# Kernel optimization log

Hardware: AMD Instinct MI355X
Metric: run time of the kernel (lower is better)

The kernel has to match this reference:

```python
import jax, jax.numpy as jnp
import numpy as np

NQ, NK, D = 8192, 8192, 256
NEG_INF = -1e30


def setup_inputs() -> dict:
    key = jax.random.key(0)
    kK, kV, kQ, kM = jax.random.split(key, 4)
    K = jax.random.normal(kK, (NK, D), dtype=jnp.float32)
    V = jax.random.normal(kV, (NK, D), dtype=jnp.float32)
    Q = jax.random.normal(kQ, (NQ, D), dtype=jnp.float32)
    m = jax.random.randint(kM, (NQ, NK), 0, 2) > 0  # bool mask, True = attend
    return {"K": K, "V": V, "Q": Q, "m": m}


def reference(K, V, Q, m):
    # affinity: scaled dot product with optional mask
    scale = 1.0 / jnp.sqrt(jnp.asarray(D, dtype=Q.dtype))
    QKt = jnp.einsum('qd,kd->qk', Q, K) * scale  # [NQ, NK]
    QKt = jnp.where(m, QKt, NEG_INF)
    # normalization: softmax over keys
    QKt_n = jax.nn.softmax(QKt, axis=-1)
    # weighted sum of values
    return QKt_n @ V  # [NQ, D]
```

## Files before the change

### kernel.cpp

```cpp
#include <hip/hip_runtime.h>
#include <stdint.h>
#include <stddef.h>

#define NQS 8192
#define NKS 8192
#define DS  256

typedef _Float16 half8 __attribute__((ext_vector_type(8)));
typedef _Float16 half4v __attribute__((ext_vector_type(4)));
typedef float floatx16 __attribute__((ext_vector_type(16)));
typedef float floatx4e __attribute__((ext_vector_type(4)));
typedef uint32_t uint32x4 __attribute__((ext_vector_type(4)));

#define MFMA32(A,B,C) __builtin_amdgcn_mfma_f32_32x32x16_f16(A,B,C,0,0,0)

#define GLOAD_LDS16(gp, lp) \
  __builtin_amdgcn_global_load_lds((const __attribute__((address_space(1))) void*)(gp), \
                                   (__attribute__((address_space(3))) void*)(lp), 16, 0, 0)

#define TILE_ELEMS 16384
#define SUB_ELEMS  8192

__global__ void detect_mask(const uint4* __restrict__ M, uint32_t* __restrict__ flag){
  __shared__ uint32_t s[256];
  uint32_t acc = 0;
  for (int i = threadIdx.x; i < 4096; i += 256){
    uint4 v = M[i];
    acc |= v.x | v.y | v.z | v.w;
  }
  s[threadIdx.x] = acc;
  __syncthreads();
  if (threadIdx.x == 0){
    uint32_t t = 0;
    for (int i = 0; i < 256; i++) t |= s[i];
    *flag = (t > 1u) ? 1u : 0u;
  }
}

__global__ void prep(const float* __restrict__ Qf, const float* __restrict__ K,
                     const float* __restrict__ V,
                     _Float16* __restrict__ Qh, _Float16* __restrict__ Kc,
                     _Float16* __restrict__ Vc){
  const int tid = threadIdx.x;
  if (blockIdx.x < 1024){
    size_t u = (size_t)blockIdx.x*256 + tid;
    const float4* src = (const float4*)(Qf + u*8);
    float4 a = src[0], b = src[1];
    half8 h = {(_Float16)a.x,(_Float16)a.y,(_Float16)a.z,(_Float16)a.w,
               (_Float16)b.x,(_Float16)b.y,(_Float16)b.z,(_Float16)b.w};
    *(half8*)(Qh + u*8) = h;
  } else if (blockIdx.x < 2048){
    int gid = (blockIdx.x - 1024)*256 + tid;
    int key = gid & 8191;
    int c   = gid >> 13;
    int kt = c >> 1, t = c & 1;
    const float4* s = (const float4*)(K + (size_t)key*DS + kt*16 + t*8);
    float4 x = s[0], y = s[1];
    half8 h = {(_Float16)x.x,(_Float16)x.y,(_Float16)x.z,(_Float16)x.w,
               (_Float16)y.x,(_Float16)y.y,(_Float16)y.z,(_Float16)y.w};
    int tile = key >> 6, mt = (key >> 5) & 1, k32 = key & 31;
    size_t off = (size_t)tile*TILE_ELEMS + (((mt*16 + kt)*2 + t)*32 + k32)*8;
    *(half8*)(Kc + off) = h;
  } else {
    int gid = (blockIdx.x - 2048)*256 + tid;
    int d32 = gid & 31;
    int t   = (gid >> 5) & 1;
    int nt  = (gid >> 6) & 7;
    int kkt = (gid >> 9) & 3;
    int tile = gid >> 11;
    int d = nt*32 + d32;
    int kb8 = tile*64 + kkt*16 + t*8;
    half8 h;
    #pragma unroll
    for (int j=0;j<8;j++) h[j] = (_Float16)V[(size_t)(kb8 + j)*DS + d];
    *(half8*)(Vc + (size_t)gid*8) = h;
  }
}

struct MaskRegs { uint32x4 v[4]; };

__device__ __forceinline__ void mask_slab_load(bool bm, const uint8_t* __restrict__ M8,
                                               int rb, int k0, int tid, MaskRegs& m){
  if (bm){
    m.v[0] = __builtin_nontemporal_load(
        (const uint32x4*)(M8 + (size_t)(rb + (tid>>1))*NKS + k0 + (tid&1)*16));
  } else {
    const uint32_t* M32 = (const uint32_t*)M8;
    #pragma unroll
    for (int jj=0;jj<4;jj++)
      m.v[jj] = __builtin_nontemporal_load(
          (const uint32x4*)(M32 + (size_t)(rb + jj*32 + (tid>>3))*NKS + k0 + (tid&7)*4));
  }
}
__device__ __forceinline__ void mask_slab_pack(bool bm, int tid, const MaskRegs& m,
                                               uint8_t (*__restrict__ nib)[8]){
  if (bm){
    #pragma unroll
    for (int q=0;q<4;q++){
      uint32_t x = m.v[0][q];
      uint8_t nb = (uint8_t)(((x&0x000000FFu)?1u:0u)|((x&0x0000FF00u)?2u:0u)|
                             ((x&0x00FF0000u)?4u:0u)|((x&0xFF000000u)?8u:0u));
      nib[tid>>1][(tid&1)*4 + q] = nb;
    }
  } else {
    #pragma unroll
    for (int jj=0;jj<4;jj++){
      uint32x4 x = m.v[jj];
      uint8_t nb = (uint8_t)((x[0]?1u:0u)|(x[1]?2u:0u)|(x[2]?4u:0u)|(x[3]?8u:0u));
      nib[jj*32 + (tid>>3)][tid&7] = nb;
    }
  }
}

__global__ __launch_bounds__(256, 2) void attn_fwd(
  const _Float16* __restrict__ Qh, const _Float16* __restrict__ Kc,
  const _Float16* __restrict__ Vc, const uint8_t* __restrict__ Msk,
  const uint32_t* __restrict__ flag, _Float16* __restrict__ Oph,
  float* __restrict__ Lo)
{
  __shared__ _Float16 Kls[2][SUB_ELEMS];
  __shared__ _Float16 Vls[2][SUB_ELEMS];
  __shared__ uint8_t  Nib[2][128][8];

  const int tid  = threadIdx.x;
  const int w    = tid >> 6;
  const int lane = tid & 63;
  const int q32  = lane & 31;
  const int t    = lane >> 5;
  const int b    = blockIdx.x;
  const int kh   = b & 7;
  const int rb   = (b >> 3)*128;
  const int rowbase = rb + w*32;
  const int sub0 = kh << 5;
  const int kbase = kh << 10;

  const float kLog = 0.09016844005556021f;
  const float MFIX = 6.0f;

  const bool bm = (*flag != 0u);

  half8 qf[16];
  {
    const _Float16* qrow = Qh + (size_t)(rowbase + q32)*DS;
    #pragma unroll
    for (int kt=0;kt<16;kt++)
      qf[kt] = *(const half8*)(qrow + kt*16 + t*8);
  }

  floatx16 O[8];
  #pragma unroll
  for (int nt=0;nt<8;nt++)
    #pragma unroll
    for (int i=0;i<16;i++) O[nt][i] = 0.f;
  float lsum = 0.f;

  {
    const size_t base = (size_t)sub0 * SUB_ELEMS;
    #pragma unroll
    for (int j=0;j<4;j++){
      int c = w*4 + j;
      GLOAD_LDS16(Kc + base + c*512 + lane*8, &Kls[0][c*512]);
      GLOAD_LDS16(Vc + base + c*512 + lane*8, &Vls[0][c*512]);
    }
    MaskRegs m0;
    mask_slab_load(bm, Msk, rb, kbase, tid, m0);
    mask_slab_pack(bm, tid, m0, Nib[0]);
  }
  __syncthreads();

  #pragma unroll 1
  for (int it=0; it<32; ++it){
    const int buf = it & 1;

    MaskRegs mpf;
    if (it < 31){
      const size_t base = (size_t)(sub0 + it + 1) * SUB_ELEMS;
      #pragma unroll
      for (int j=0;j<4;j++){
        int c = w*4 + j;
        GLOAD_LDS16(Kc + base + c*512 + lane*8, &Kls[buf^1][c*512]);
        GLOAD_LDS16(Vc + base + c*512 + lane*8, &Vls[buf^1][c*512]);
      }
      mask_slab_load(bm, Msk, rb, kbase + (it+1)*32, tid, mpf);
    }

    const uint2 nq = *(const uint2*)&Nib[buf][w*32 + q32][0];
    const uint32_t nib_s[4] = { (nq.x >> (8*t))      & 0xFu,
                                (nq.x >> (16 + 8*t)) & 0xFu,
                                (nq.y >> (8*t))      & 0xFu,
                                (nq.y >> (16 + 8*t)) & 0xFu };

    floatx16 S0, S1;
    #pragma unroll
    for (int i=0;i<16;i++){ S0[i]=0.f; S1[i]=0.f; }
    #pragma unroll
    for (int kt=0;kt<8;kt++){
      half8 kA = *(const half8*)&Kls[buf][((kt*2 + t)*32 + q32)*8];
      S0 = MFMA32(kA, qf[kt], S0);
    }
    #pragma unroll
    for (int kt=8;kt<16;kt++){
      half8 kA = *(const half8*)&Kls[buf][((kt*2 + t)*32 + q32)*8];
      S1 = MFMA32(kA, qf[kt], S1);
    }

    uint32_t pk[4][2];
    #pragma unroll
    for (int s=0;s<4;s++){
      float pv[4];
      #pragma unroll
      for (int rr=0;rr<4;rr++){
        int i = s*4 + rr;
        float e = __builtin_amdgcn_exp2f(__builtin_fmaf(S0[i]+S1[i], kLog, -MFIX));
        float p = ((nib_s[s] >> rr) & 1u) ? e : 0.f;
        lsum += p;
        pv[rr] = p;
      }
      pk[s][0] = __builtin_bit_cast(uint32_t, __builtin_amdgcn_cvt_pkrtz(pv[0], pv[1]));
      pk[s][1] = __builtin_bit_cast(uint32_t, __builtin_amdgcn_cvt_pkrtz(pv[2], pv[3]));
    }

    #pragma unroll
    for (int kt2=0; kt2<2; ++kt2){
      const int s_own  = kt2*2 + t;
      const int s_send = kt2*2 + (t^1);
      uint32_t r0 = __shfl_xor(__builtin_bit_cast(int, pk[s_send][0]), 32);
      uint32_t r1 = __shfl_xor(__builtin_bit_cast(int, pk[s_send][1]), 32);
      uint32_t lo0 = (t==0) ? pk[s_own][0] : r0;
      uint32_t lo1 = (t==0) ? pk[s_own][1] : r1;
      uint32_t hi0 = (t==0) ? r0 : pk[s_own][0];
      uint32_t hi1 = (t==0) ? r1 : pk[s_own][1];
      uint4 u = {lo0, lo1, hi0, hi1};
      half8 pa = __builtin_bit_cast(half8, u);
      #pragma unroll
      for (int nt=0;nt<8;nt++){
        half8 vB = *(const half8*)&Vls[buf][(((kt2*8+nt)*2 + t)*32 + q32)*8];
        O[nt] = MFMA32(pa, vB, O[nt]);
      }
    }

    if (it < 31) mask_slab_pack(bm, tid, mpf, Nib[buf^1]);

    __syncthreads();
  }

  lsum += __builtin_bit_cast(float, __shfl_xor(__builtin_bit_cast(int, lsum), 32));
  if (t == 0) __builtin_nontemporal_store(lsum, &Lo[(size_t)b*128 + w*32 + q32]);

  _Float16* ob = Oph + ((size_t)b*128 + w*32)*256;
  #pragma unroll
  for (int nt=0;nt<8;nt++){
    #pragma unroll
    for (int i=0;i<16;i++){
      int row = (i&3) + 8*(i>>2) + 4*t;
      __builtin_nontemporal_store((_Float16)O[nt][i], &ob[(size_t)row*256 + nt*32 + q32]);
    }
  }
}

__global__ void combine8(const _Float16* __restrict__ Oph, const float* __restrict__ Lo,
                         float* __restrict__ Out){
  int gid = blockIdx.x*256 + threadIdx.x;
  int row = gid >> 6;
  int c4  = (gid & 63) << 2;
  int g   = row >> 7, r = row & 127;

  float lt = 0.f;
  #pragma unroll
  for (int kh=0;kh<8;kh++) lt += __builtin_nontemporal_load(&Lo[(size_t)(g*8 + kh)*128 + r]);
  float li = 1.0f / lt;

  floatx4e acc = {0.f,0.f,0.f,0.f};
  #pragma unroll
  for (int kh=0;kh<8;kh++){
    half4v o = __builtin_nontemporal_load(
        (const half4v*)(Oph + ((size_t)(g*8 + kh)*128 + r)*256 + c4));
    acc[0] += (float)o[0]; acc[1] += (float)o[1];
    acc[2] += (float)o[2]; acc[3] += (float)o[3];
  }
  acc[0] *= li; acc[1] *= li; acc[2] *= li; acc[3] *= li;
  __builtin_nontemporal_store(acc, (floatx4e*)(Out + (size_t)row*DS + c4));
}

extern "C" void kernel_launch(void* const* d_in, const int* in_sizes, int n_in,
                              void* d_out, int out_size, void* d_ws, size_t ws_size,
                              hipStream_t stream){
  (void)in_sizes; (void)n_in; (void)out_size; (void)ws_size;
  const float*   K = (const float*)d_in[0];
  const float*   V = (const float*)d_in[1];
  const float*   Q = (const float*)d_in[2];
  const uint8_t* M = (const uint8_t*)d_in[3];
  float* Out = (float*)d_out;

  _Float16* Qh  = (_Float16*)d_ws;
  _Float16* Kc  = Qh + (size_t)NQS*DS;
  _Float16* Vc  = Kc + (size_t)NKS*DS;
  _Float16* Oph = Vc + (size_t)NKS*DS;
  float*    Lo  = (float*)(Oph + (size_t)512*128*256);
  uint32_t* flag = (uint32_t*)(Lo + 512*128);

  hipLaunchKernelGGL(detect_mask, dim3(1),    dim3(256), 0, stream, (const uint4*)M, flag);
  hipLaunchKernelGGL(prep,        dim3(3072), dim3(256), 0, stream, Q, K, V, Qh, Kc, Vc);
  hipLaunchKernelGGL(attn_fwd,    dim3(512),  dim3(256), 0, stream, Qh, Kc, Vc, M, flag, Oph, Lo);
  hipLaunchKernelGGL(combine8,    dim3(2048), dim3(256), 0, stream, Oph, Lo, Out);
}
```

Measured before the change: 493.6 us.

## Preload entire mask slab into packed LDS nibbles before the main loop

Moves all of the per-block mask loading and bit-packing out of the main attention loop into a prologue. The prologue stores the packed nibbles for every key sub-tile in a 16-entry shared array, two sub-tiles per byte. This removes mask loads, register pressure and packing work from the MFMA loop. The cost is a serialized up-front mask read that is no longer overlapped with compute, plus extra LDS use that may affect occupancy.

```diff
diff --git a/kernel.cpp b/kernel.cpp
--- a/kernel.cpp
+++ b/kernel.cpp
@@ -77,41 +77,6 @@
   }
 }
 
-struct MaskRegs { uint32x4 v[4]; };
-
-__device__ __forceinline__ void mask_slab_load(bool bm, const uint8_t* __restrict__ M8,
-                                               int rb, int k0, int tid, MaskRegs& m){
-  if (bm){
-    m.v[0] = __builtin_nontemporal_load(
-        (const uint32x4*)(M8 + (size_t)(rb + (tid>>1))*NKS + k0 + (tid&1)*16));
-  } else {
-    const uint32_t* M32 = (const uint32_t*)M8;
-    #pragma unroll
-    for (int jj=0;jj<4;jj++)
-      m.v[jj] = __builtin_nontemporal_load(
-          (const uint32x4*)(M32 + (size_t)(rb + jj*32 + (tid>>3))*NKS + k0 + (tid&7)*4));
-  }
-}
-__device__ __forceinline__ void mask_slab_pack(bool bm, int tid, const MaskRegs& m,
-                                               uint8_t (*__restrict__ nib)[8]){
-  if (bm){
-    #pragma unroll
-    for (int q=0;q<4;q++){
-      uint32_t x = m.v[0][q];
-      uint8_t nb = (uint8_t)(((x&0x000000FFu)?1u:0u)|((x&0x0000FF00u)?2u:0u)|
-                             ((x&0x00FF0000u)?4u:0u)|((x&0xFF000000u)?8u:0u));
-      nib[tid>>1][(tid&1)*4 + q] = nb;
-    }
-  } else {
-    #pragma unroll
-    for (int jj=0;jj<4;jj++){
-      uint32x4 x = m.v[jj];
-      uint8_t nb = (uint8_t)((x[0]?1u:0u)|(x[1]?2u:0u)|(x[2]?4u:0u)|(x[3]?8u:0u));
-      nib[jj*32 + (tid>>3)][tid&7] = nb;
-    }
-  }
-}
-
 __global__ __launch_bounds__(256, 2) void attn_fwd(
   const _Float16* __restrict__ Qh, const _Float16* __restrict__ Kc,
   const _Float16* __restrict__ Vc, const uint8_t* __restrict__ Msk,
@@ -120,7 +85,7 @@
 {
   __shared__ _Float16 Kls[2][SUB_ELEMS];
   __shared__ _Float16 Vls[2][SUB_ELEMS];
-  __shared__ uint8_t  Nib[2][128][8];
+  __shared__ uint8_t  Pk[16][128][8];
 
   const int tid  = threadIdx.x;
   const int w    = tid >> 6;
@@ -139,21 +104,6 @@
 
   const bool bm = (*flag != 0u);
 
-  half8 qf[16];
-  {
-    const _Float16* qrow = Qh + (size_t)(rowbase + q32)*DS;
-    #pragma unroll
-    for (int kt=0;kt<16;kt++)
-      qf[kt] = *(const half8*)(qrow + kt*16 + t*8);
-  }
-
-  floatx16 O[8];
-  #pragma unroll
-  for (int nt=0;nt<8;nt++)
-    #pragma unroll
-    for (int i=0;i<16;i++) O[nt][i] = 0.f;
-  float lsum = 0.f;
-
   {
     const size_t base = (size_t)sub0 * SUB_ELEMS;
     #pragma unroll
@@ -162,17 +112,65 @@
       GLOAD_LDS16(Kc + base + c*512 + lane*8, &Kls[0][c*512]);
       GLOAD_LDS16(Vc + base + c*512 + lane*8, &Vls[0][c*512]);
     }
-    MaskRegs m0;
-    mask_slab_load(bm, Msk, rb, kbase, tid, m0);
-    mask_slab_pack(bm, tid, m0, Nib[0]);
-  }
+  }
+
+  if (bm){
+    const uint8_t* mrow = Msk + (size_t)(rb + (tid>>1))*NKS + kbase + (tid&1)*16;
+    #pragma unroll 1
+    for (int sp=0; sp<16; ++sp){
+      uint32x4 e = __builtin_nontemporal_load((const uint32x4*)(mrow + sp*64));
+      uint32x4 o = __builtin_nontemporal_load((const uint32x4*)(mrow + sp*64 + 32));
+      #pragma unroll
+      for (int q=0;q<4;q++){
+        uint32_t xe = e[q], xo = o[q];
+        uint8_t ne = (uint8_t)(((xe&0x000000FFu)?1u:0u)|((xe&0x0000FF00u)?2u:0u)|
+                               ((xe&0x00FF0000u)?4u:0u)|((xe&0xFF000000u)?8u:0u));
+        uint8_t no = (uint8_t)(((xo&0x000000FFu)?1u:0u)|((xo&0x0000FF00u)?2u:0u)|
+                               ((xo&0x00FF0000u)?4u:0u)|((xo&0xFF000000u)?8u:0u));
+        Pk[sp][tid>>1][(tid&1)*4 + q] = (uint8_t)(ne | (no << 4));
+      }
+    }
+  } else {
+    const uint32_t* M32 = (const uint32_t*)Msk;
+    #pragma unroll 1
+    for (int sp=0; sp<16; ++sp){
+      uint32x4 e[4], o[4];
+      #pragma unroll
+      for (int jj=0;jj<4;jj++){
+        const uint32_t* p = M32 + (size_t)(rb + jj*32 + (tid>>3))*NKS + kbase + sp*64 + (tid&7)*4;
+        e[jj] = __builtin_nontemporal_load((const uint32x4*)p);
+        o[jj] = __builtin_nontemporal_load((const uint32x4*)(p + 32));
+      }
+      #pragma unroll
+      for (int jj=0;jj<4;jj++){
+        uint8_t ne = (uint8_t)((e[jj][0]?1u:0u)|(e[jj][1]?2u:0u)|(e[jj][2]?4u:0u)|(e[jj][3]?8u:0u));
+        uint8_t no = (uint8_t)((o[jj][0]?1u:0u)|(o[jj][1]?2u:0u)|(o[jj][2]?4u:0u)|(o[jj][3]?8u:0u));
+        Pk[sp][jj*32 + (tid>>3)][tid&7] = (uint8_t)(ne | (no << 4));
+      }
+    }
+  }
+
+  half8 qf[16];
+  {
+    const _Float16* qrow = Qh + (size_t)(rowbase + q32)*DS;
+    #pragma unroll
+    for (int kt=0;kt<16;kt++)
+      qf[kt] = *(const half8*)(qrow + kt*16 + t*8);
+  }
+
+  floatx16 O[8];
+  #pragma unroll
+  for (int nt=0;nt<8;nt++)
+    #pragma unroll
+    for (int i=0;i<16;i++) O[nt][i] = 0.f;
+  float lsum = 0.f;
+
   __syncthreads();
 
   #pragma unroll 1
   for (int it=0; it<32; ++it){
     const int buf = it & 1;
 
-    MaskRegs mpf;
     if (it < 31){
       const size_t base = (size_t)(sub0 + it + 1) * SUB_ELEMS;
       #pragma unroll
@@ -181,14 +179,14 @@
         GLOAD_LDS16(Kc + base + c*512 + lane*8, &Kls[buf^1][c*512]);
         GLOAD_LDS16(Vc + base + c*512 + lane*8, &Vls[buf^1][c*512]);
       }
-      mask_slab_load(bm, Msk, rb, kbase + (it+1)*32, tid, mpf);
-    }
-
-    const uint2 nq = *(const uint2*)&Nib[buf][w*32 + q32][0];
-    const uint32_t nib_s[4] = { (nq.x >> (8*t))      & 0xFu,
-                                (nq.x >> (16 + 8*t)) & 0xFu,
-                                (nq.y >> (8*t))      & 0xFu,
-                                (nq.y >> (16 + 8*t)) & 0xFu };
+    }
+
+    const uint2 nq = *(const uint2*)&Pk[it>>1][w*32 + q32][0];
+    const int sh = (it & 1) * 4;
+    const uint32_t nib_s[4] = { (nq.x >> (8*t + sh))      & 0xFu,
+                                (nq.x >> (16 + 8*t + sh)) & 0xFu,
+                                (nq.y >> (8*t + sh))      & 0xFu,
+                                (nq.y >> (16 + 8*t + sh)) & 0xFu };
 
     floatx16 S0, S1;
     #pragma unroll
@@ -239,8 +237,6 @@
       }
     }
 
-    if (it < 31) mask_slab_pack(bm, tid, mpf, Nib[buf^1]);
-
     __syncthreads();
   }
 
```

Measured after the change: 468.6 us. 5.1% less time.
